# Kernel tuning notes

Hardware: AMD Instinct MI355X
Metric: run time of the kernel (lower is better)

Reference implementation:

```python
import jax, jax.numpy as jnp
import numpy as np

N = 50000      # nodes
E = 800000     # edges per relation
R = 2          # relations
L = 2          # conv layers
D = 128        # hidden / input channels
G = 64         # graphs in batch
C = 8          # num_classes


def setup_inputs() -> dict:
    key = jax.random.key(0)
    ks = jax.random.split(key, 6)
    x = jax.random.normal(ks[0], (N, D), dtype=jnp.float32)
    W = jax.random.normal(ks[1], (L, R, D, D), dtype=jnp.float32) * 0.05
    b = jnp.zeros((L, R, D), dtype=jnp.float32)
    lin_w = jax.random.normal(ks[2], (D, C), dtype=jnp.float32) * 0.05
    lin_b = jnp.zeros((C,), dtype=jnp.float32)
    edge_index = jax.random.randint(ks[3], (R, 2, E), 0, N, dtype=jnp.int32)
    batch = jnp.sort(jax.random.randint(ks[4], (N,), 0, G, dtype=jnp.int32))
    return {"x": x, "W": W, "b": b, "lin_w": lin_w, "lin_b": lin_b,
            "edge_index": edge_index, "batch": batch}


def _gcn_conv(x, src, dst, inv_sqrt_deg, W_r, b_r):
    """PyG GCNConv: symmetric-normalized aggregation with self loops.
    out[i] = sum_{j->i} d_i^-1/2 d_j^-1/2 (x_j W) + d_i^-1 (x_i W) + b
    where d includes the self loop (in-degree + 1)."""
    xw = x @ W_r                                   # [N, D]
    norm = inv_sqrt_deg[src] * inv_sqrt_deg[dst]   # [E]
    agg = jax.ops.segment_sum(xw[src] * norm[:, None], dst, num_segments=N)
    agg = agg + xw * (inv_sqrt_deg * inv_sqrt_deg)[:, None]  # self-loop msg
    return agg + b_r


def reference(x, W, b, lin_w, lin_b, edge_index, batch):
    # Pre-compute per-relation symmetric normalization (same for all layers).
    inv_sqrt_degs = []
    for r in range(R):
        dst = edge_index[r, 1]
        deg = jax.ops.segment_sum(jnp.ones((E,), x.dtype), dst, num_segments=N) + 1.0
        inv_sqrt_degs.append(jax.lax.rsqrt(deg))

    h = x
    for l in range(L):
        out = jnp.zeros((N, D), x.dtype)
        for r in range(R):  # HeteroConv aggr='sum' over relations
            out = out + _gcn_conv(h, edge_index[r, 0], edge_index[r, 1],
                                  inv_sqrt_degs[r], W[l, r], b[l, r])
        h = jax.nn.relu(out) if l < L - 1 else out

    # global_mean_pool over batch ids
    counts = jax.ops.segment_sum(jnp.ones((N,), x.dtype), batch, num_segments=G)
    sums = jax.ops.segment_sum(h, batch, num_segments=G)
    pooled = sums / jnp.maximum(counts, 1.0)[:, None]   # [G, D]
    # dropout(p=0.5) is identity in eval mode; final Linear
    return pooled @ lin_w + lin_b                        # [G, C]
```

## Files before the change

### kernel.cpp

```cpp
#include <hip/hip_runtime.h>
#include <math.h>

#define NN 50000
#define EE 800000
#define RR 2
#define LL 2
#define DD 128
#define GG 64
#define CCLS 8
#define NBUK 196
#define BCAP 6144

typedef unsigned int uint;
typedef unsigned short ushort;
typedef short bf16x8 __attribute__((ext_vector_type(8)));
typedef float f32x4 __attribute__((ext_vector_type(4)));
typedef float f32x2 __attribute__((ext_vector_type(2)));

#define OFF_XW    ((size_t)0)
#define OFF_H1    ((size_t)12800000)
#define OFF_WBT   ((size_t)25600000)
#define OFF_ISD   ((size_t)25731072)
#define OFF_RP    ((size_t)26131072)
#define OFF_CI    ((size_t)26531136)
#define OFF_BD    ((size_t)32931136)
#define OFF_ZERO  ((size_t)42564928)
#define ZO_GCUR 0
#define ZO_SUM  1600
#define ZO_CNT  34368
#define ZERO_BYTES 34624

static __device__ __forceinline__ ushort f2b(float f) {
  uint u = __float_as_uint(f);
  uint r = (u + 0x7fffu + ((u >> 16) & 1u)) >> 16;
  return (ushort)r;
}
static __device__ __forceinline__ float blo(uint u) { return __uint_as_float(u << 16); }
static __device__ __forceinline__ float bhi(uint u) { return __uint_as_float(u & 0xffff0000u); }

__global__ __launch_bounds__(256) void k_wprep(const float* __restrict__ W,
                                               ushort* __restrict__ WT) {
  int idx = blockIdx.x * 256 + threadIdx.x;
  int lr = idx >> 14;
  int rem = idx & 16383;
  int n = rem >> 7, k = rem & 127;
  WT[lr * 16384 + n * 128 + k] = f2b(W[lr * 16384 + k * 128 + n]);
}

__global__ __launch_bounds__(256) void k_part(const int* __restrict__ EI,
                                              int* __restrict__ gcur,
                                              uint* __restrict__ bdata) {
  __shared__ int hist[256];
  __shared__ int sbase[256];
  __shared__ int gbase[256];
  __shared__ int lcur[256];
  __shared__ uint stage[4096];
  __shared__ unsigned char bstage[4096];
  const int r = blockIdx.y;
  const int t = threadIdx.x;
  const int e0 = blockIdx.x * 4096;
  const int cnt = min(4096, EE - e0);
  hist[t] = 0;
  lcur[t] = 0;
  __syncthreads();

  int src[16], dst[16];
  bool val[4];
#pragma unroll
  for (int j = 0; j < 4; ++j) {
    int i4 = (j * 256 + t) * 4;
    val[j] = (i4 < cnt);
    if (val[j]) {
      int4 s4 = *(const int4*)(EI + (size_t)r * 2 * EE + e0 + i4);
      int4 d4 = *(const int4*)(EI + (size_t)r * 2 * EE + EE + e0 + i4);
      src[j * 4 + 0] = s4.x; src[j * 4 + 1] = s4.y; src[j * 4 + 2] = s4.z; src[j * 4 + 3] = s4.w;
      dst[j * 4 + 0] = d4.x; dst[j * 4 + 1] = d4.y; dst[j * 4 + 2] = d4.z; dst[j * 4 + 3] = d4.w;
#pragma unroll
      for (int i = 0; i < 4; ++i) atomicAdd(&hist[dst[j * 4 + i] >> 8], 1);
    }
  }
  __syncthreads();
  int hv = hist[t];
  if (t < NBUK && hv > 0)
    gbase[t] = atomicAdd(&gcur[r * NBUK + t], hv);
  else
    gbase[t] = 0;
  sbase[t] = hv;
  __syncthreads();
  for (int off = 1; off < 256; off <<= 1) {
    int u = (t >= off) ? sbase[t - off] : 0;
    __syncthreads();
    sbase[t] += u;
    __syncthreads();
  }
  int incl = sbase[t];
  hist[t] = incl - hv;
  __syncthreads();
#pragma unroll
  for (int j = 0; j < 4; ++j) {
    if (val[j]) {
#pragma unroll
      for (int i = 0; i < 4; ++i) {
        int d = dst[j * 4 + i];
        int b = d >> 8;
        int p = atomicAdd(&lcur[b], 1);
        int pos = hist[b] + p;
        stage[pos] = ((uint)src[j * 4 + i] << 8) | (uint)(d & 255);
        bstage[pos] = (unsigned char)b;
      }
    }
  }
  __syncthreads();
  for (int s = t; s < cnt; s += 256) {
    int b = (int)bstage[s];
    bdata[(size_t)(r * NBUK + b) * BCAP + gbase[b] + (s - hist[b])] = stage[s];
  }
}

__global__ __launch_bounds__(256) void k_csr(const uint* __restrict__ bdata,
                                             const int* __restrict__ gcur,
                                             float* __restrict__ isd,
                                             int* __restrict__ rp,
                                             int* __restrict__ ci) {
  __shared__ int lcnt[256];
  __shared__ int lrp[256];
  __shared__ int lcur[256];
  __shared__ int cstage[BCAP];
  __shared__ int basesh;
  const int b = blockIdx.x;
  const int r = blockIdx.y;
  const int t = threadIdx.x;
  const int cnt = gcur[r * NBUK + b];
  lcnt[t] = (t < b) ? gcur[r * NBUK + t] : 0;
  __syncthreads();
  for (int off = 128; off > 0; off >>= 1) {
    if (t < off) lcnt[t] += lcnt[t + off];
    __syncthreads();
  }
  if (t == 0) basesh = lcnt[0];
  __syncthreads();
  const int base = basesh;
  const uint* bd = bdata + (size_t)(r * NBUK + b) * BCAP;
  __syncthreads();
  lcnt[t] = 0;
  lcur[t] = 0;
  __syncthreads();
  for (int s = t; s < cnt; s += 256) {
    uint pr = bd[s];
    atomicAdd(&lcnt[pr & 255u], 1);
  }
  __syncthreads();
  int deg = lcnt[t];
  lrp[t] = deg;
  __syncthreads();
  for (int off = 1; off < 256; off <<= 1) {
    int u = (t >= off) ? lrp[t - off] : 0;
    __syncthreads();
    lrp[t] += u;
    __syncthreads();
  }
  int incl = lrp[t];
  __syncthreads();
  lrp[t] = incl - deg;
  __syncthreads();
  int node = b * 256 + t;
  if (node < NN) {
    isd[r * NN + node] = rsqrtf((float)(deg + 1));
    rp[r * (NN + 1) + node] = base + lrp[t];
  }
  if (b == NBUK - 1 && t == 0) rp[r * (NN + 1) + NN] = EE;
  for (int s = t; s < cnt; s += 256) {
    uint pr = bd[s];
    int j = (int)(pr & 255u);
    int p = atomicAdd(&lcur[j], 1);
    cstage[lrp[j] + p] = (int)(pr >> 8);
  }
  __syncthreads();
  for (int s = t; s < cnt; s += 256) ci[(size_t)r * EE + base + s] = cstage[s];
}

#define AL_S 72
#define WT_S 136
template <int IN_BF16>
__global__ __launch_bounds__(256) void k_gemm(const void* __restrict__ Xv,
                                              const ushort* __restrict__ WTg,
                                              uint* __restrict__ Y) {
  __shared__ ushort WTl[128 * WT_S];
  __shared__ ushort Al[128 * AL_S];
  const int r = blockIdx.y;
  const int m0b = blockIdx.x * 128;
  const int t = threadIdx.x;
  const int w = t >> 6, L = t & 63, q = L >> 4, ln = L & 15;
  uint* Yr = Y + (size_t)r * NN * 32;
  const ushort* WTr = WTg + (size_t)r * 16384;

#pragma unroll
  for (int i = 0; i < 8; ++i) {
    int g = t + i * 256;
    int n = g >> 4, k0 = (g & 15) * 8;
    *(uint4*)(&WTl[n * WT_S + k0]) = *(const uint4*)(WTr + n * 128 + k0);
  }

  f32x4 acc[2][8];
#pragma unroll
  for (int mt = 0; mt < 2; ++mt)
#pragma unroll
    for (int nt = 0; nt < 8; ++nt) {
      acc[mt][nt][0] = 0.f; acc[mt][nt][1] = 0.f;
      acc[mt][nt][2] = 0.f; acc[mt][nt][3] = 0.f;
    }

  for (int hh = 0; hh < 2; ++hh) {
    __syncthreads();
    {
      int row = t >> 1, ch = t & 1;
      int gm = m0b + row;
      ushort* dst = &Al[row * AL_S + ch * 32];
      if (gm < NN) {
        if (IN_BF16) {
          const uint4* xp = (const uint4*)((const ushort*)Xv + (size_t)gm * 128 + hh * 64 + ch * 32);
#pragma unroll
          for (int j = 0; j < 4; ++j) ((uint4*)dst)[j] = xp[j];
        } else {
          const float4* xp = (const float4*)((const float*)Xv + (size_t)gm * 128 + hh * 64 + ch * 32);
          ushort tmp[32];
#pragma unroll
          for (int j = 0; j < 8; ++j) {
            float4 v = xp[j];
            tmp[j * 4 + 0] = f2b(v.x); tmp[j * 4 + 1] = f2b(v.y);
            tmp[j * 4 + 2] = f2b(v.z); tmp[j * 4 + 3] = f2b(v.w);
          }
#pragma unroll
          for (int j = 0; j < 4; ++j) ((uint4*)dst)[j] = ((uint4*)tmp)[j];
        }
      } else {
        uint4 z = make_uint4(0, 0, 0, 0);
#pragma unroll
        for (int j = 0; j < 4; ++j) ((uint4*)dst)[j] = z;
      }
    }
    __syncthreads();
#pragma unroll
    for (int kk = 0; kk < 2; ++kk) {
      bf16x8 b0 = *(const bf16x8*)(&Al[(w * 32 + ln) * AL_S + kk * 32 + q * 8]);
      bf16x8 b1 = *(const bf16x8*)(&Al[(w * 32 + 16 + ln) * AL_S + kk * 32 + q * 8]);
#pragma unroll
      for (int nt = 0; nt < 8; ++nt) {
        bf16x8 a = *(const bf16x8*)(&WTl[(nt * 16 + ln) * WT_S + hh * 64 + kk * 32 + q * 8]);
        acc[0][nt] = __builtin_amdgcn_mfma_f32_16x16x32_bf16(a, b0, acc[0][nt], 0, 0, 0);
        acc[1][nt] = __builtin_amdgcn_mfma_f32_16x16x32_bf16(a, b1, acc[1][nt], 0, 0, 0);
      }
    }
  }
#pragma unroll
  for (int mt = 0; mt < 2; ++mt) {
    int m = m0b + w * 32 + mt * 16 + ln;
    if (m < NN) {
      uint* yp = Yr + (size_t)m * 32;
#pragma unroll
      for (int nt = 0; nt < 8; ++nt) {
        f32x4 v = acc[mt][nt];
        uint u = __builtin_amdgcn_cvt_pk_fp8_f32(v[0], v[1], 0u, false);
        u = __builtin_amdgcn_cvt_pk_fp8_f32(v[2], v[3], u, true);
        yp[nt * 4 + q] = u;
      }
    }
  }
}

__global__ __launch_bounds__(256) void k_agg(const ushort* __restrict__ xw,
                                             const int* __restrict__ rp,
                                             const int* __restrict__ ci,
                                             const float* __restrict__ isd,
                                             const float* __restrict__ bias,
                                             uint* __restrict__ hout, int relu_flag) {
  int w = threadIdx.x >> 6;
  int lane = threadIdx.x & 63;
  int i = blockIdx.x * 4 + w;
  float aLo = bias[lane * 2] + bias[DD + lane * 2];
  float aHi = bias[lane * 2 + 1] + bias[DD + lane * 2 + 1];
#pragma unroll
  for (int r = 0; r < RR; ++r) {
    const ushort* xwr = xw + (size_t)r * NN * 64;
    const float* isdr = isd + r * NN;
    const int* cir = ci + (size_t)r * EE;
    float di = isdr[i];
    {
      f32x2 v = __builtin_amdgcn_cvt_pk_f32_fp8((uint)xwr[(size_t)i * 64 + lane], false);
      float dd = di * di;
      aLo += v[0] * dd;
      aHi += v[1] * dd;
    }
    int e0 = rp[r * (NN + 1) + i];
    int e1 = rp[r * (NN + 1) + i + 1];
    int e = e0;
    for (; e + 8 <= e1; e += 8) {
      int s[8];
      uint u[8];
      float wt[8];
#pragma unroll
      for (int j = 0; j < 8; ++j) s[j] = cir[e + j];
#pragma unroll
      for (int j = 0; j < 8; ++j) u[j] = (uint)xwr[(size_t)s[j] * 64 + lane];
#pragma unroll
      for (int j = 0; j < 8; ++j) wt[j] = isdr[s[j]] * di;
#pragma unroll
      for (int j = 0; j < 8; ++j) {
        f32x2 v = __builtin_amdgcn_cvt_pk_f32_fp8(u[j], false);
        aLo += v[0] * wt[j];
        aHi += v[1] * wt[j];
      }
    }
    for (; e < e1; ++e) {
      int s = cir[e];
      float wt = isdr[s] * di;
      f32x2 v = __builtin_amdgcn_cvt_pk_f32_fp8((uint)xwr[(size_t)s * 64 + lane], false);
      aLo += v[0] * wt;
      aHi += v[1] * wt;
    }
  }
  if (relu_flag) {
    aLo = fmaxf(aLo, 0.f);
    aHi = fmaxf(aHi, 0.f);
  }
  hout[(size_t)i * 64 + lane] = (uint)f2b(aLo) | ((uint)f2b(aHi) << 16);
}

#define PCHUNK 32
__global__ __launch_bounds__(64) void k_pool(const uint* __restrict__ h,
                                             const int* __restrict__ batch,
                                             float* __restrict__ sums,
                                             int* __restrict__ counts) {
  int lane = threadIdx.x;
  int n0 = blockIdx.x * PCHUNK;
  int n1 = n0 + PCHUNK;
  if (n1 > NN) n1 = NN;
  if (n0 >= NN) return;
  float aLo = 0.f, aHi = 0.f;
  int cnt = 0;
  int g = batch[n0];
  uint u = h[(size_t)n0 * 64 + lane];
  for (int n = n0; n < n1; ++n) {
    uint unext = 0;
    int gnext = g;
    if (n + 1 < n1) {
      unext = h[(size_t)(n + 1) * 64 + lane];
      gnext = batch[n + 1];
    }
    aLo += blo(u);
    aHi += bhi(u);
    cnt++;
    if (n + 1 < n1 && gnext != g) {
      atomicAdd(&sums[g * DD + lane * 2], aLo);
      atomicAdd(&sums[g * DD + lane * 2 + 1], aHi);
      if (lane == 0) atomicAdd(&counts[g], cnt);
      aLo = 0.f; aHi = 0.f; cnt = 0;
      g = gnext;
    }
    u = unext;
  }
  atomicAdd(&sums[g * DD + lane * 2], aLo);
  atomicAdd(&sums[g * DD + lane * 2 + 1], aHi);
  if (lane == 0) atomicAdd(&counts[g], cnt);
}

__global__ __launch_bounds__(512) void k_final(const float* __restrict__ sums,
                                               const int* __restrict__ counts,
                                               const float* __restrict__ lin_w,
                                               const float* __restrict__ lin_b,
                                               float* __restrict__ out) {
  int t = threadIdx.x;
  int g = t >> 3, co = t & 7;
  float cnt = (float)counts[g];
  if (cnt < 1.f) cnt = 1.f;
  float inv = 1.f / cnt;
  float v = lin_b[co];
  for (int d = 0; d < DD; ++d) v += (sums[g * DD + d] * inv) * lin_w[d * CCLS + co];
  out[t] = v;
}

extern "C" void kernel_launch(void* const* d_in, const int* in_sizes, int n_in,
                              void* d_out, int out_size, void* d_ws, size_t ws_size,
                              hipStream_t stream) {
  (void)in_sizes; (void)n_in; (void)out_size; (void)ws_size;
  const float* x     = (const float*)d_in[0];
  const float* W     = (const float*)d_in[1];
  const float* b     = (const float*)d_in[2];
  const float* lin_w = (const float*)d_in[3];
  const float* lin_b = (const float*)d_in[4];
  const int*   EI    = (const int*)d_in[5];
  const int*   batch = (const int*)d_in[6];
  float* out = (float*)d_out;

  char* ws = (char*)d_ws;
  uint*   xw    = (uint*)(ws + OFF_XW);
  uint*   h1    = (uint*)(ws + OFF_H1);
  ushort* WbfT  = (ushort*)(ws + OFF_WBT);
  float*  isd   = (float*)(ws + OFF_ISD);
  int*    rp    = (int*)(ws + OFF_RP);
  int*    ci    = (int*)(ws + OFF_CI);
  uint*   bdata = (uint*)(ws + OFF_BD);
  char*   zb    = ws + OFF_ZERO;
  int*    gcur  = (int*)(zb + ZO_GCUR);
  float*  sums  = (float*)(zb + ZO_SUM);
  int*    counts= (int*)(zb + ZO_CNT);

  (void)hipMemsetAsync(zb, 0, ZERO_BYTES, stream);

  k_wprep<<<256, 256, 0, stream>>>(W, WbfT);
  k_part<<<dim3((EE + 4095) / 4096, RR), 256, 0, stream>>>(EI, gcur, bdata);
  k_csr<<<dim3(NBUK, RR), 256, 0, stream>>>(bdata, gcur, isd, rp, ci);

  for (int l = 0; l < LL; ++l) {
    const ushort* WTl_g = WbfT + (size_t)l * RR * DD * DD;
    if (l == 0)
      k_gemm<0><<<dim3((NN + 127) / 128, RR), 256, 0, stream>>>((const void*)x, WTl_g, xw);
    else
      k_gemm<1><<<dim3((NN + 127) / 128, RR), 256, 0, stream>>>((const void*)h1, WTl_g, xw);
    k_agg<<<(NN + 3) / 4, 256, 0, stream>>>((const ushort*)xw, rp, ci, isd,
                                            b + (size_t)l * RR * DD, h1,
                                            (l < LL - 1) ? 1 : 0);
  }
  k_pool<<<(NN + PCHUNK - 1) / PCHUNK, 64, 0, stream>>>(h1, batch, sums, counts);
  k_final<<<1, GG * CCLS, 0, stream>>>(sums, counts, lin_w, lin_b, out);
}
```

Before: 297.7 us.

## Prescale GEMM output by source degree and gather fp8 rows eight edges per wave

The GEMM epilogue now multiplies each row by its source inverse-sqrt degree before fp8 packing, so aggregation no longer needs a per-edge isd gather or per-edge weight multiply; the destination factor is applied once per relation. The aggregation kernel is restructured so each wave processes 8 edges at once, with each 8-lane group loading a 16-byte fp8 chunk, index prefetch for the next batch, and a cross-group shuffle reduction at the end. The self-loop is folded into the edge loop as an extra source. This aims to cut dependent gather latency and the isd traffic, at the cost of more registers and shuffle reductions, and it changes fp8 rounding because scaling now happens before quantisation.

```diff
diff --git a/kernel.cpp b/kernel.cpp
--- a/kernel.cpp
+++ b/kernel.cpp
@@ -184,6 +184,7 @@
 template <int IN_BF16>
 __global__ __launch_bounds__(256) void k_gemm(const void* __restrict__ Xv,
                                               const ushort* __restrict__ WTg,
+                                              const float* __restrict__ isd,
                                               uint* __restrict__ Y) {
   __shared__ ushort WTl[128 * WT_S];
   __shared__ ushort Al[128 * AL_S];
@@ -256,74 +257,96 @@
   for (int mt = 0; mt < 2; ++mt) {
     int m = m0b + w * 32 + mt * 16 + ln;
     if (m < NN) {
+      float sc = isd[r * NN + m];
       uint* yp = Yr + (size_t)m * 32;
 #pragma unroll
       for (int nt = 0; nt < 8; ++nt) {
         f32x4 v = acc[mt][nt];
-        uint u = __builtin_amdgcn_cvt_pk_fp8_f32(v[0], v[1], 0u, false);
-        u = __builtin_amdgcn_cvt_pk_fp8_f32(v[2], v[3], u, true);
+        uint u = __builtin_amdgcn_cvt_pk_fp8_f32(v[0] * sc, v[1] * sc, 0u, false);
+        u = __builtin_amdgcn_cvt_pk_fp8_f32(v[2] * sc, v[3] * sc, u, true);
         yp[nt * 4 + q] = u;
       }
     }
   }
 }
 
-__global__ __launch_bounds__(256) void k_agg(const ushort* __restrict__ xw,
+__global__ __launch_bounds__(256) void k_agg(const uint4* __restrict__ xw4,
                                              const int* __restrict__ rp,
                                              const int* __restrict__ ci,
                                              const float* __restrict__ isd,
                                              const float* __restrict__ bias,
                                              uint* __restrict__ hout, int relu_flag) {
-  int w = threadIdx.x >> 6;
-  int lane = threadIdx.x & 63;
-  int i = blockIdx.x * 4 + w;
-  float aLo = bias[lane * 2] + bias[DD + lane * 2];
-  float aHi = bias[lane * 2 + 1] + bias[DD + lane * 2 + 1];
+  const int w = threadIdx.x >> 6;
+  const int lane = threadIdx.x & 63;
+  const int g = lane >> 3, c = lane & 7;
+  const int i = blockIdx.x * 4 + w;
+
+  float tot[16];
+#pragma unroll
+  for (int k = 0; k < 16; ++k) tot[k] = 0.f;
+
 #pragma unroll
   for (int r = 0; r < RR; ++r) {
-    const ushort* xwr = xw + (size_t)r * NN * 64;
-    const float* isdr = isd + r * NN;
+    const uint4* xwr = xw4 + (size_t)r * NN * 8;
     const int* cir = ci + (size_t)r * EE;
-    float di = isdr[i];
-    {
-      f32x2 v = __builtin_amdgcn_cvt_pk_f32_fp8((uint)xwr[(size_t)i * 64 + lane], false);
-      float dd = di * di;
-      aLo += v[0] * dd;
-      aHi += v[1] * dd;
-    }
-    int e0 = rp[r * (NN + 1) + i];
-    int e1 = rp[r * (NN + 1) + i + 1];
-    int e = e0;
-    for (; e + 8 <= e1; e += 8) {
-      int s[8];
-      uint u[8];
-      float wt[8];
-#pragma unroll
-      for (int j = 0; j < 8; ++j) s[j] = cir[e + j];
-#pragma unroll
-      for (int j = 0; j < 8; ++j) u[j] = (uint)xwr[(size_t)s[j] * 64 + lane];
-#pragma unroll
-      for (int j = 0; j < 8; ++j) wt[j] = isdr[s[j]] * di;
-#pragma unroll
-      for (int j = 0; j < 8; ++j) {
-        f32x2 v = __builtin_amdgcn_cvt_pk_f32_fp8(u[j], false);
-        aLo += v[0] * wt[j];
-        aHi += v[1] * wt[j];
+    const float di = isd[r * NN + i];
+    const int e0 = rp[r * (NN + 1) + i];
+    const int cnt = rp[r * (NN + 1) + i + 1] - e0;
+    const int total = cnt + 1;
+
+    float acc[16];
+#pragma unroll
+    for (int k = 0; k < 16; ++k) acc[k] = 0.f;
+
+    int s_cur = (g < cnt) ? cir[e0 + g] : i;
+    for (int base = 0; base < total; base += 8) {
+      int idxn = base + 8 + g;
+      int s_next = (idxn < cnt) ? cir[e0 + idxn] : i;
+      if (base + g < total) {
+        uint4 u = xwr[(size_t)s_cur * 8 + c];
+        f32x2 v;
+        v = __builtin_amdgcn_cvt_pk_f32_fp8(u.x, false); acc[0] += v[0];  acc[1] += v[1];
+        v = __builtin_amdgcn_cvt_pk_f32_fp8(u.x, true);  acc[2] += v[0];  acc[3] += v[1];
+        v = __builtin_amdgcn_cvt_pk_f32_fp8(u.y, false); acc[4] += v[0];  acc[5] += v[1];
+        v = __builtin_amdgcn_cvt_pk_f32_fp8(u.y, true);  acc[6] += v[0];  acc[7] += v[1];
+        v = __builtin_amdgcn_cvt_pk_f32_fp8(u.z, false); acc[8] += v[0];  acc[9] += v[1];
+        v = __builtin_amdgcn_cvt_pk_f32_fp8(u.z, true);  acc[10] += v[0]; acc[11] += v[1];
+        v = __builtin_amdgcn_cvt_pk_f32_fp8(u.w, false); acc[12] += v[0]; acc[13] += v[1];
+        v = __builtin_amdgcn_cvt_pk_f32_fp8(u.w, true);  acc[14] += v[0]; acc[15] += v[1];
       }
-    }
-    for (; e < e1; ++e) {
-      int s = cir[e];
-      float wt = isdr[s] * di;
-      f32x2 v = __builtin_amdgcn_cvt_pk_f32_fp8((uint)xwr[(size_t)s * 64 + lane], false);
-      aLo += v[0] * wt;
-      aHi += v[1] * wt;
-    }
-  }
-  if (relu_flag) {
-    aLo = fmaxf(aLo, 0.f);
-    aHi = fmaxf(aHi, 0.f);
-  }
-  hout[(size_t)i * 64 + lane] = (uint)f2b(aLo) | ((uint)f2b(aHi) << 16);
+      s_cur = s_next;
+    }
+#pragma unroll
+    for (int k = 0; k < 16; ++k) tot[k] = fmaf(di, acc[k], tot[k]);
+  }
+
+#pragma unroll
+  for (int mask = 8; mask <= 32; mask <<= 1) {
+#pragma unroll
+    for (int k = 0; k < 16; ++k) tot[k] += __shfl_xor(tot[k], mask);
+  }
+
+  if (g < 2) {
+    int ch0 = c * 16 + g * 8;
+    const float4* bp = (const float4*)(bias + ch0);
+    const float4* bq = (const float4*)(bias + DD + ch0);
+    float4 b0 = bp[0], b1 = bp[1], b2 = bq[0], b3 = bq[1];
+    float o[8];
+#pragma unroll
+    for (int j = 0; j < 8; ++j) o[j] = (g == 0) ? tot[j] : tot[8 + j];
+    o[0] += b0.x + b2.x; o[1] += b0.y + b2.y; o[2] += b0.z + b2.z; o[3] += b0.w + b2.w;
+    o[4] += b1.x + b3.x; o[5] += b1.y + b3.y; o[6] += b1.z + b3.z; o[7] += b1.w + b3.w;
+    if (relu_flag) {
+#pragma unroll
+      for (int j = 0; j < 8; ++j) o[j] = fmaxf(o[j], 0.f);
+    }
+    uint4 pk;
+    pk.x = (uint)f2b(o[0]) | ((uint)f2b(o[1]) << 16);
+    pk.y = (uint)f2b(o[2]) | ((uint)f2b(o[3]) << 16);
+    pk.z = (uint)f2b(o[4]) | ((uint)f2b(o[5]) << 16);
+    pk.w = (uint)f2b(o[6]) | ((uint)f2b(o[7]) << 16);
+    ((uint4*)(hout + (size_t)i * 64))[c * 2 + g] = pk;
+  }
 }
 
 #define PCHUNK 32
@@ -414,10 +437,10 @@
   for (int l = 0; l < LL; ++l) {
     const ushort* WTl_g = WbfT + (size_t)l * RR * DD * DD;
     if (l == 0)
-      k_gemm<0><<<dim3((NN + 127) / 128, RR), 256, 0, stream>>>((const void*)x, WTl_g, xw);
+      k_gemm<0><<<dim3((NN + 127) / 128, RR), 256, 0, stream>>>((const void*)x, WTl_g, isd, xw);
     else
-      k_gemm<1><<<dim3((NN + 127) / 128, RR), 256, 0, stream>>>((const void*)h1, WTl_g, xw);
-    k_agg<<<(NN + 3) / 4, 256, 0, stream>>>((const ushort*)xw, rp, ci, isd,
+      k_gemm<1><<<dim3((NN + 127) / 128, RR), 256, 0, stream>>>((const void*)h1, WTl_g, isd, xw);
+    k_agg<<<(NN + 3) / 4, 256, 0, stream>>>((const uint4*)xw, rp, ci, isd,
                                             b + (size_t)l * RR * DD, h1,
                                             (l < LL - 1) ? 1 : 0);
   }
```

New measurement: 257.0 us. -13.7%, faster.
